# Optimization experiments

Measured on AMD Instinct MI355X. Metric: run time of the kernel, lower is better.

## Reference

```python
import jax, jax.numpy as jnp
import numpy as np

B, IN, OUT = 1024, 512, 64000
EPS = 1e-12  # matches torch F.normalize eps


def setup_inputs() -> dict:
    key = jax.random.key(0)
    k1, k2, k3 = jax.random.split(key, 3)
    x = jax.random.normal(k1, (B, IN), dtype=jnp.float32)
    label = jax.random.randint(k2, (B,), 0, OUT)
    # xavier_uniform_ for weight [OUT, IN]: limit = sqrt(6 / (fan_in + fan_out))
    limit = float(np.sqrt(6.0 / (IN + OUT)))
    weight = jax.random.uniform(k3, (OUT, IN), dtype=jnp.float32, minval=-limit, maxval=limit)
    s = 50               # python scalar; set via _calculate_para but UNUSED in normfree output
    m = jnp.full((1,), 0.5, dtype=jnp.float32)  # margin
    return {"x": x, "label": label, "weight": weight, "s": s, "m": m}


def reference(x, label, weight, s, m):
    m = m.reshape(())
    cos_m, sin_m = jnp.cos(m), jnp.sin(m)
    # norm of raw input (the 'normfree' scale replacing s)
    norm = jnp.linalg.norm(x, axis=1, keepdims=True)            # [B, 1]
    xn = x / jnp.maximum(norm, EPS)                             # F.normalize(input)
    wn = weight / jnp.maximum(
        jnp.linalg.norm(weight, axis=1, keepdims=True), EPS)    # F.normalize(weight)
    cosine = xn @ wn.T                                          # [B, OUT]
    sine = jnp.sqrt(jnp.clip(1.0 - cosine * cosine, 0.0, None))
    phi = cosine * cos_m - sine * sin_m                         # cos(theta + m)
    # per-sample loop in torch == one-hot substitution only where cosine > 0
    onehot = jax.nn.one_hot(label, OUT, dtype=bool)             # [B, OUT]
    mod_cosine = jnp.where(onehot & (cosine > 0), phi, cosine)
    return norm * mod_cosine, wn
```

## Files before the change

kernel.cpp:

```cpp
#include <hip/hip_runtime.h>
#include <cstdint>

#define EPSN 1e-12f
static constexpr int B_ROWS = 1024;
static constexpr int IN_DIM = 512;
static constexpr int OUT_DIM = 64000;

typedef __attribute__((ext_vector_type(8))) short bf16x8;
typedef __attribute__((ext_vector_type(4))) float f32x4;

__device__ __forceinline__ unsigned short f2bf(float f) {
  uint32_t u = __builtin_bit_cast(uint32_t, f);
  u += 0x7fffu + ((u >> 16) & 1u);
  return (unsigned short)(u >> 16);
}

__device__ __forceinline__ float bf2f(unsigned short h) {
  uint32_t u = (uint32_t)h << 16;
  return __builtin_bit_cast(float, u);
}

__device__ __forceinline__ float wave_sum(float v) {
#pragma unroll
  for (int off = 32; off; off >>= 1) v += __shfl_xor(v, off);
  return v;
}

__device__ __forceinline__ void async16(const void* g, void* l) {
  __builtin_amdgcn_global_load_lds((const __attribute__((address_space(1))) uint32_t*)g,
                                   (__attribute__((address_space(3))) uint32_t*)l, 16, 0, 0);
}

__global__ void prep_kernel(const float* __restrict__ X, const int* __restrict__ label,
                            const float* __restrict__ Wg, float* __restrict__ norms,
                            float* __restrict__ fixdot, unsigned short* __restrict__ xbf) {
  int lane = threadIdx.x & 63;
  int row = blockIdx.x * 4 + (threadIdx.x >> 6);
  const float* src = X + (size_t)row * IN_DIM + lane * 8;
  float4 a = *(const float4*)src;
  float4 b = *(const float4*)(src + 4);
  uint4 u;
  u.x = (uint32_t)f2bf(a.x) | ((uint32_t)f2bf(a.y) << 16);
  u.y = (uint32_t)f2bf(a.z) | ((uint32_t)f2bf(a.w) << 16);
  u.z = (uint32_t)f2bf(b.x) | ((uint32_t)f2bf(b.y) << 16);
  u.w = (uint32_t)f2bf(b.z) | ((uint32_t)f2bf(b.w) << 16);
  *(uint4*)(xbf + (size_t)row * IN_DIM + lane * 8) = u;
  float ssx = a.x * a.x;
  ssx = fmaf(a.y, a.y, ssx); ssx = fmaf(a.z, a.z, ssx); ssx = fmaf(a.w, a.w, ssx);
  ssx = fmaf(b.x, b.x, ssx); ssx = fmaf(b.y, b.y, ssx); ssx = fmaf(b.z, b.z, ssx);
  ssx = fmaf(b.w, b.w, ssx);
  int lab = label[row];
  const float* wsrc = Wg + (size_t)lab * IN_DIM + lane * 8;
  float4 wa = *(const float4*)wsrc, wb = *(const float4*)(wsrc + 4);
  float d = a.x * wa.x;
  d = fmaf(a.y, wa.y, d); d = fmaf(a.z, wa.z, d); d = fmaf(a.w, wa.w, d);
  d = fmaf(b.x, wb.x, d); d = fmaf(b.y, wb.y, d); d = fmaf(b.z, wb.z, d);
  d = fmaf(b.w, wb.w, d);
  float ssw = wa.x * wa.x;
  ssw = fmaf(wa.y, wa.y, ssw); ssw = fmaf(wa.z, wa.z, ssw); ssw = fmaf(wa.w, wa.w, ssw);
  ssw = fmaf(wb.x, wb.x, ssw); ssw = fmaf(wb.y, wb.y, ssw); ssw = fmaf(wb.z, wb.z, ssw);
  ssw = fmaf(wb.w, wb.w, ssw);
  ssx = wave_sum(ssx);
  d = wave_sum(d);
  ssw = wave_sum(ssw);
  if (lane == 0) {
    norms[row] = sqrtf(ssx);
    fixdot[row] = d / fmaxf(sqrtf(ssw), EPSN);
  }
}

__global__ void wcast_kernel(const float* __restrict__ Wg, unsigned short* __restrict__ wbf) {
  int lane = threadIdx.x & 63;
  int row = blockIdx.x * 4 + (threadIdx.x >> 6);
  const float* src = Wg + (size_t)row * IN_DIM + lane * 8;
  float4 a = *(const float4*)src;
  float4 b = *(const float4*)(src + 4);
  float ss = a.x * a.x;
  ss = fmaf(a.y, a.y, ss); ss = fmaf(a.z, a.z, ss); ss = fmaf(a.w, a.w, ss);
  ss = fmaf(b.x, b.x, ss); ss = fmaf(b.y, b.y, ss); ss = fmaf(b.z, b.z, ss);
  ss = fmaf(b.w, b.w, ss);
  ss = wave_sum(ss);
  float inv = 1.0f / fmaxf(sqrtf(ss), EPSN);
  uint4 u;
  u.x = (uint32_t)f2bf(a.x * inv) | ((uint32_t)f2bf(a.y * inv) << 16);
  u.y = (uint32_t)f2bf(a.z * inv) | ((uint32_t)f2bf(a.w * inv) << 16);
  u.z = (uint32_t)f2bf(b.x * inv) | ((uint32_t)f2bf(b.y * inv) << 16);
  u.w = (uint32_t)f2bf(b.z * inv) | ((uint32_t)f2bf(b.w * inv) << 16);
  *(uint4*)(wbf + (size_t)row * IN_DIM + lane * 8) = u;
}

__global__ __launch_bounds__(512, 2) void gemm_epi_kernel(
    const unsigned short* __restrict__ Abf, const unsigned short* __restrict__ Bbf,
    const float* __restrict__ norms, const float* __restrict__ fixdot,
    const int* __restrict__ label, const float* __restrict__ mArr,
    float* __restrict__ out0, float* __restrict__ wnOut) {
  __shared__ char smem[65536];

  const int t = threadIdx.x;
  int flat = blockIdx.x;
  int xcd = flat & 7;
  int wk = (flat >> 3) + xcd * 500;
  int mT = wk & 7, nT = wk >> 3;
  int rowA0 = mT * 128, rowB0 = nT * 128;

  int lane = t & 63;
  int wid = t >> 6;
  int wm = wid >> 1, wn2 = wid & 1;
  int rl = lane & 15, sl = lane >> 4;

  int r0 = t >> 2, q0 = (t & 3) ^ ((r0 >> 1) & 3);
  const unsigned short* aP = Abf + (size_t)(rowA0 + r0) * IN_DIM + q0 * 8;
  const unsigned short* bP = Bbf + (size_t)(rowB0 + r0) * IN_DIM + q0 * 8;

  auto issueSub = [&](int sig) {
    int kcol = sig * 32;
    char* aD = smem + (sig & 3) * 8192;
    char* bD = smem + 32768 + (sig & 3) * 8192;
    async16(aP + kcol, aD + t * 16);
    async16(bP + kcol, bD + t * 16);
  };

  issueSub(0); issueSub(1); issueSub(2);

  f32x4 acc[2][4];
#pragma unroll
  for (int m = 0; m < 2; ++m)
#pragma unroll
    for (int n = 0; n < 4; ++n) acc[m][n] = (f32x4){0.f, 0.f, 0.f, 0.f};

#pragma unroll 1
  for (int sigma = 0; sigma < 16; ++sigma) {
    __builtin_amdgcn_sched_barrier(0);
    if (sigma <= 13)      asm volatile("s_waitcnt vmcnt(4)" ::: "memory");
    else if (sigma == 14) asm volatile("s_waitcnt vmcnt(2)" ::: "memory");
    else                  asm volatile("s_waitcnt vmcnt(0)" ::: "memory");
    __builtin_amdgcn_s_barrier();
    __builtin_amdgcn_sched_barrier(0);

    const char* aB = smem + (sigma & 3) * 8192;
    const char* bB = smem + 32768 + (sigma & 3) * 8192;
    bf16x8 av[2], bv[4];
#pragma unroll
    for (int m = 0; m < 2; ++m) {
      int r = wm * 32 + m * 16 + rl;
      av[m] = *(const bf16x8*)(aB + r * 64 + ((sl ^ ((r >> 1) & 3)) * 16));
    }
#pragma unroll
    for (int n = 0; n < 4; ++n) {
      int r = wn2 * 64 + n * 16 + rl;
      bv[n] = *(const bf16x8*)(bB + r * 64 + ((sl ^ ((r >> 1) & 3)) * 16));
    }
    if (sigma + 3 <= 15) issueSub(sigma + 3);
    __builtin_amdgcn_s_setprio(1);
#pragma unroll
    for (int n = 0; n < 4; ++n)
#pragma unroll
      for (int m = 0; m < 2; ++m)
        acc[m][n] = __builtin_amdgcn_mfma_f32_16x16x32_bf16(av[m], bv[n], acc[m][n], 0, 0, 0);
    __builtin_amdgcn_s_setprio(0);
    asm volatile("s_waitcnt lgkmcnt(0)" ::: "memory");
    __builtin_amdgcn_s_barrier();
    __builtin_amdgcn_sched_barrier(0);
  }

  {
    int r = t >> 5;
    int c = (t & 31) * 16;
    int row = rowB0 + mT * 16 + r;
    const unsigned short* srcp = Bbf + (size_t)row * IN_DIM + c;
    uint4 u0 = *(const uint4*)srcp;
    uint4 u1 = *(const uint4*)(srcp + 8);
    float* dst = wnOut + (size_t)row * IN_DIM + c;
    float4 f;
    f.x = bf2f((unsigned short)(u0.x & 0xffff)); f.y = bf2f((unsigned short)(u0.x >> 16));
    f.z = bf2f((unsigned short)(u0.y & 0xffff)); f.w = bf2f((unsigned short)(u0.y >> 16));
    *(float4*)dst = f;
    f.x = bf2f((unsigned short)(u0.z & 0xffff)); f.y = bf2f((unsigned short)(u0.z >> 16));
    f.z = bf2f((unsigned short)(u0.w & 0xffff)); f.w = bf2f((unsigned short)(u0.w >> 16));
    *(float4*)(dst + 4) = f;
    f.x = bf2f((unsigned short)(u1.x & 0xffff)); f.y = bf2f((unsigned short)(u1.x >> 16));
    f.z = bf2f((unsigned short)(u1.y & 0xffff)); f.w = bf2f((unsigned short)(u1.y >> 16));
    *(float4*)(dst + 8) = f;
    f.x = bf2f((unsigned short)(u1.z & 0xffff)); f.y = bf2f((unsigned short)(u1.z >> 16));
    f.z = bf2f((unsigned short)(u1.w & 0xffff)); f.w = bf2f((unsigned short)(u1.w >> 16));
    *(float4*)(dst + 12) = f;
  }

  float mm = mArr[0];
  float cm = cosf(mm), sm = sinf(mm);
  int rowb = rowA0 + wm * 32, colb = rowB0 + wn2 * 64;
#pragma unroll
  for (int m = 0; m < 2; ++m) {
#pragma unroll
    for (int q = 0; q < 4; ++q) {
      int R = rowb + m * 16 + sl * 4 + q;
      int lab = label[R];
      float nv = norms[R], fv = fixdot[R];
      float* orow = out0 + (size_t)R * OUT_DIM;
#pragma unroll
      for (int n = 0; n < 4; ++n) {
        int Cc = colb + n * 16 + rl;
        float val = acc[m][n][q];
        if (Cc == lab) {
          float c = fv / fmaxf(nv, EPSN);
          val = (c > 0.f) ? nv * (c * cm - sqrtf(fmaxf(1.f - c * c, 0.f)) * sm) : fv;
        }
        orow[Cc] = val;
      }
    }
  }
}

extern "C" void kernel_launch(void* const* d_in, const int* in_sizes, int n_in,
                              void* d_out, int out_size, void* d_ws, size_t ws_size,
                              hipStream_t stream) {
  const float* x = (const float*)d_in[0];
  const int* label = (const int*)d_in[1];
  const float* weight = (const float*)d_in[2];
  const float* mArr = (const float*)d_in[4];

  float* out0 = (float*)d_out;
  float* wnOut = out0 + (size_t)B_ROWS * OUT_DIM;

  char* ws = (char*)d_ws;
  float* norms = (float*)ws;
  float* fixdot = (float*)(ws + 4096);
  unsigned short* xbf = (unsigned short*)(ws + 8192);
  unsigned short* wbf = (unsigned short*)(ws + 8192 + 2ull * B_ROWS * IN_DIM);

  prep_kernel<<<B_ROWS / 4, 256, 0, stream>>>(x, label, weight, norms, fixdot, xbf);
  wcast_kernel<<<OUT_DIM / 4, 256, 0, stream>>>(weight, wbf);
  gemm_epi_kernel<<<4000, 512, 0, stream>>>(xbf, wbf, norms, fixdot, label, mArr,
                                            out0, wnOut);
}
```

Baseline: 230.0 us.

## Enlarge GEMM block tile to 256x256 and trim per-iteration barrier

```diff
diff --git a/kernel.cpp b/kernel.cpp
--- a/kernel.cpp
+++ b/kernel.cpp
@@ -94,55 +94,61 @@
     const float* __restrict__ norms, const float* __restrict__ fixdot,
     const int* __restrict__ label, const float* __restrict__ mArr,
     float* __restrict__ out0, float* __restrict__ wnOut) {
-  __shared__ char smem[65536];
+  __shared__ char smem[131072];
 
   const int t = threadIdx.x;
   int flat = blockIdx.x;
   int xcd = flat & 7;
-  int wk = (flat >> 3) + xcd * 500;
-  int mT = wk & 7, nT = wk >> 3;
-  int rowA0 = mT * 128, rowB0 = nT * 128;
+  int wk = (flat >> 3) + xcd * 125;
+  int mT = wk & 3, nT = wk >> 2;
+  int rowA0 = mT * 256, rowB0 = nT * 256;
 
   int lane = t & 63;
   int wid = t >> 6;
-  int wm = wid >> 1, wn2 = wid & 1;
+  int wm = wid >> 2, wn2 = wid & 3;
   int rl = lane & 15, sl = lane >> 4;
 
   int r0 = t >> 2, q0 = (t & 3) ^ ((r0 >> 1) & 3);
-  const unsigned short* aP = Abf + (size_t)(rowA0 + r0) * IN_DIM + q0 * 8;
-  const unsigned short* bP = Bbf + (size_t)(rowB0 + r0) * IN_DIM + q0 * 8;
+  int r1 = (t + 512) >> 2, q1 = ((t + 512) & 3) ^ ((r1 >> 1) & 3);
+  const unsigned short* aP0 = Abf + (size_t)(rowA0 + r0) * IN_DIM + q0 * 8;
+  const unsigned short* aP1 = Abf + (size_t)(rowA0 + r1) * IN_DIM + q1 * 8;
+  const unsigned short* bP0 = Bbf + (size_t)(rowB0 + r0) * IN_DIM + q0 * 8;
+  const unsigned short* bP1 = Bbf + (size_t)(rowB0 + r1) * IN_DIM + q1 * 8;
 
   auto issueSub = [&](int sig) {
     int kcol = sig * 32;
-    char* aD = smem + (sig & 3) * 8192;
-    char* bD = smem + 32768 + (sig & 3) * 8192;
-    async16(aP + kcol, aD + t * 16);
-    async16(bP + kcol, bD + t * 16);
+    char* aD = smem + (sig & 3) * 16384;
+    char* bD = smem + 65536 + (sig & 3) * 16384;
+    async16(aP0 + kcol, aD + t * 16);
+    async16(aP1 + kcol, aD + (t + 512) * 16);
+    async16(bP0 + kcol, bD + t * 16);
+    async16(bP1 + kcol, bD + (t + 512) * 16);
   };
 
   issueSub(0); issueSub(1); issueSub(2);
 
-  f32x4 acc[2][4];
-#pragma unroll
-  for (int m = 0; m < 2; ++m)
+  f32x4 acc[8][4];
+#pragma unroll
+  for (int m = 0; m < 8; ++m)
 #pragma unroll
     for (int n = 0; n < 4; ++n) acc[m][n] = (f32x4){0.f, 0.f, 0.f, 0.f};
 
 #pragma unroll 1
   for (int sigma = 0; sigma < 16; ++sigma) {
     __builtin_amdgcn_sched_barrier(0);
-    if (sigma <= 13)      asm volatile("s_waitcnt vmcnt(4)" ::: "memory");
-    else if (sigma == 14) asm volatile("s_waitcnt vmcnt(2)" ::: "memory");
+    if (sigma <= 13)      asm volatile("s_waitcnt vmcnt(8)" ::: "memory");
+    else if (sigma == 14) asm volatile("s_waitcnt vmcnt(4)" ::: "memory");
     else                  asm volatile("s_waitcnt vmcnt(0)" ::: "memory");
     __builtin_amdgcn_s_barrier();
     __builtin_amdgcn_sched_barrier(0);
-
-    const char* aB = smem + (sigma & 3) * 8192;
-    const char* bB = smem + 32768 + (sigma & 3) * 8192;
-    bf16x8 av[2], bv[4];
-#pragma unroll
-    for (int m = 0; m < 2; ++m) {
-      int r = wm * 32 + m * 16 + rl;
+    if (sigma + 3 <= 15) issueSub(sigma + 3);
+
+    const char* aB = smem + (sigma & 3) * 16384;
+    const char* bB = smem + 65536 + (sigma & 3) * 16384;
+    bf16x8 av[8], bv[4];
+#pragma unroll
+    for (int m = 0; m < 8; ++m) {
+      int r = wm * 128 + m * 16 + rl;
       av[m] = *(const bf16x8*)(aB + r * 64 + ((sl ^ ((r >> 1) & 3)) * 16));
     }
 #pragma unroll
@@ -150,47 +156,39 @@
       int r = wn2 * 64 + n * 16 + rl;
       bv[n] = *(const bf16x8*)(bB + r * 64 + ((sl ^ ((r >> 1) & 3)) * 16));
     }
-    if (sigma + 3 <= 15) issueSub(sigma + 3);
     __builtin_amdgcn_s_setprio(1);
 #pragma unroll
     for (int n = 0; n < 4; ++n)
 #pragma unroll
-      for (int m = 0; m < 2; ++m)
+      for (int m = 0; m < 8; ++m)
         acc[m][n] = __builtin_amdgcn_mfma_f32_16x16x32_bf16(av[m], bv[n], acc[m][n], 0, 0, 0);
     __builtin_amdgcn_s_setprio(0);
-    asm volatile("s_waitcnt lgkmcnt(0)" ::: "memory");
-    __builtin_amdgcn_s_barrier();
-    __builtin_amdgcn_sched_barrier(0);
   }
 
   {
-    int r = t >> 5;
-    int c = (t & 31) * 16;
-    int row = rowB0 + mT * 16 + r;
-    const unsigned short* srcp = Bbf + (size_t)row * IN_DIM + c;
-    uint4 u0 = *(const uint4*)srcp;
-    uint4 u1 = *(const uint4*)(srcp + 8);
-    float* dst = wnOut + (size_t)row * IN_DIM + c;
-    float4 f;
-    f.x = bf2f((unsigned short)(u0.x & 0xffff)); f.y = bf2f((unsigned short)(u0.x >> 16));
-    f.z = bf2f((unsigned short)(u0.y & 0xffff)); f.w = bf2f((unsigned short)(u0.y >> 16));
-    *(float4*)dst = f;
-    f.x = bf2f((unsigned short)(u0.z & 0xffff)); f.y = bf2f((unsigned short)(u0.z >> 16));
-    f.z = bf2f((unsigned short)(u0.w & 0xffff)); f.w = bf2f((unsigned short)(u0.w >> 16));
-    *(float4*)(dst + 4) = f;
-    f.x = bf2f((unsigned short)(u1.x & 0xffff)); f.y = bf2f((unsigned short)(u1.x >> 16));
-    f.z = bf2f((unsigned short)(u1.y & 0xffff)); f.w = bf2f((unsigned short)(u1.y >> 16));
-    *(float4*)(dst + 8) = f;
-    f.x = bf2f((unsigned short)(u1.z & 0xffff)); f.y = bf2f((unsigned short)(u1.z >> 16));
-    f.z = bf2f((unsigned short)(u1.w & 0xffff)); f.w = bf2f((unsigned short)(u1.w >> 16));
-    *(float4*)(dst + 12) = f;
+    int r = t >> 3;
+    int c0 = (t & 7) * 64;
+    int row = rowB0 + mT * 64 + r;
+    const unsigned short* srcp = Bbf + (size_t)row * IN_DIM + c0;
+    float* dst = wnOut + (size_t)row * IN_DIM + c0;
+#pragma unroll
+    for (int g = 0; g < 8; ++g) {
+      uint4 uu = *(const uint4*)(srcp + g * 8);
+      float4 f;
+      f.x = bf2f((unsigned short)(uu.x & 0xffff)); f.y = bf2f((unsigned short)(uu.x >> 16));
+      f.z = bf2f((unsigned short)(uu.y & 0xffff)); f.w = bf2f((unsigned short)(uu.y >> 16));
+      *(float4*)(dst + g * 8) = f;
+      f.x = bf2f((unsigned short)(uu.z & 0xffff)); f.y = bf2f((unsigned short)(uu.z >> 16));
+      f.z = bf2f((unsigned short)(uu.w & 0xffff)); f.w = bf2f((unsigned short)(uu.w >> 16));
+      *(float4*)(dst + g * 8 + 4) = f;
+    }
   }
 
   float mm = mArr[0];
   float cm = cosf(mm), sm = sinf(mm);
-  int rowb = rowA0 + wm * 32, colb = rowB0 + wn2 * 64;
-#pragma unroll
-  for (int m = 0; m < 2; ++m) {
+  int rowb = rowA0 + wm * 128, colb = rowB0 + wn2 * 64;
+#pragma unroll
+  for (int m = 0; m < 8; ++m) {
 #pragma unroll
     for (int q = 0; q < 4; ++q) {
       int R = rowb + m * 16 + sl * 4 + q;
@@ -230,6 +228,6 @@
 
   prep_kernel<<<B_ROWS / 4, 256, 0, stream>>>(x, label, weight, norms, fixdot, xbf);
   wcast_kernel<<<OUT_DIM / 4, 256, 0, stream>>>(weight, wbf);
-  gemm_epi_kernel<<<4000, 512, 0, stream>>>(xbf, wbf, norms, fixdot, label, mArr,
+  gemm_epi_kernel<<<1000, 512, 0, stream>>>(xbf, wbf, norms, fixdot, label, mArr,
                                             out0, wnOut);
 }
```

New measurement: 209.1 us. -9.1%, faster.
